# Optimization experiments

Measured on AMD Instinct MI355X. Metric: run time of the kernel, lower is better.

The kernel has to match this reference:

```python
import jax, jax.numpy as jnp
import numpy as np

NUM_CODES = 8192
LATENT_DIM = 256
BETA = 0.25
EPS_NORM = 1e-12  # F.normalize eps


def setup_inputs() -> dict:
    key = jax.random.key(0)
    k1, k2 = jax.random.split(key)
    z = jax.random.normal(k1, (8, LATENT_DIM, 32, 32), dtype=jnp.float32)
    # embedding initialized uniform(-1/K, 1/K); use that scale for realism
    codebook = jax.random.uniform(k2, (NUM_CODES, LATENT_DIM), dtype=jnp.float32,
                                  minval=-1.0 / NUM_CODES, maxval=1.0 / NUM_CODES)
    return {"z": z, "codebook": codebook}


def reference(z, codebook):
    # forward re-normalizes the codebook rows (F.normalize dim=1)
    norm = jnp.sqrt(jnp.sum(codebook * codebook, axis=1, keepdims=True))
    w = codebook / jnp.maximum(norm, EPS_NORM)                      # [K, D]

    z_perm = jnp.transpose(z, (0, 2, 3, 1))                          # [B, H, W, D]
    B, H, W, D = z_perm.shape
    zf = z_perm.reshape(-1, D)                                       # [N, D]

    # squared euclidean distances: ||z||^2 + ||w||^2 - 2 z w^T
    d = (jnp.sum(zf * zf, axis=1, keepdims=True)
         + jnp.sum(w * w, axis=1)
         - 2.0 * jnp.einsum('nd,kd->nk', zf, w))                     # [N, K]
    idx = jnp.argmin(d, axis=1)                                      # [N] int

    z_q = w[idx].reshape(B, H, W, D)                                 # gather

    # commitment + codebook loss
    loss = (jnp.mean((jax.lax.stop_gradient(z_q) - z_perm) ** 2)
            + BETA * jnp.mean((z_q - jax.lax.stop_gradient(z_perm)) ** 2))

    # straight-through estimator
    z_q = z_perm + jax.lax.stop_gradient(z_q - z_perm)

    # perplexity from codeword usage histogram (== mean of one-hots)
    N = idx.shape[0]
    counts = jnp.zeros((NUM_CODES,), dtype=jnp.float32).at[idx].add(1.0)
    avg_probs = counts / N
    perplexity = jnp.exp(-jnp.sum(avg_probs * jnp.log(avg_probs + 1e-10)))

    z_q = jnp.transpose(z_q, (0, 3, 1, 2))                           # back to NCHW
    return (z_q, idx, loss, perplexity)
```

## Files before the change

kernel.cpp:

```cpp
#include <hip/hip_runtime.h>
#include <hip/hip_bf16.h>
#include <math.h>

#define KC 8192
#define DD 256
#define NP 8192
#define ZQ_ELEMS 2097152
#define MARGIN_S 2.5e-4f
#define NPART 32

#define OFF_ABIG 0u
#define OFF_BBIG 8388608u
#define OFF_NRM  16777216u
#define OFF_WSQ  16809984u
#define OFF_ZSQ  16842752u
#define OFF_PV1  16875520u
#define OFF_PV2  17924096u
#define OFF_PK1  18972672u
#define OFF_LOSSP 20021248u
#define OFF_IDX  20025344u
#define OFF_FLAG 20058112u
#define OFF_HIST 20090880u
#define OFF_PACK 20123648u
#define OFF_LIST 20189184u
#define OFF_NFLG 20221952u

typedef __attribute__((ext_vector_type(8))) short bf16x8;
typedef __attribute__((ext_vector_type(4))) float f32x4;
typedef __attribute__((address_space(3))) void as3_void;
typedef const __attribute__((address_space(1))) void as1_cvoid;

#define GLOAD16(g, l) __builtin_amdgcn_global_load_lds((as1_cvoid*)(g), (as3_void*)(l), 16, 0, 0)

__device__ inline double waveReduceD(double v) {
#pragma unroll
    for (int off = 32; off; off >>= 1) v += __shfl_down(v, off, 64);
    return v;
}

static __device__ inline unsigned short f2bf(float f) {
    __hip_bfloat16 h = __float2bfloat16(f);
    return *(unsigned short*)&h;
}
static __device__ inline float bf2f(unsigned short u) {
    unsigned v = ((unsigned)u) << 16;
    float f;
    __builtin_memcpy(&f, &v, 4);
    return f;
}

__global__ __launch_bounds__(256) void prep(
    const float* __restrict__ cb, const float* __restrict__ z,
    unsigned short* __restrict__ Bbig, unsigned short* __restrict__ Abig,
    float* __restrict__ nrm, float* __restrict__ wsq, float* __restrict__ zsq,
    int* __restrict__ hist, int* __restrict__ nflag) {
    __shared__ double lred[4];
    __shared__ float mh;
    int bid = blockIdx.x, t = threadIdx.x;
    int lane = t & 63, wid = t >> 6;
    if (bid < KC) {
        int k = bid;
        if (k < 32) hist[k * 256 + t] = 0;
        if (k == 32 && t == 0) *nflag = 0;
        float c = cb[k * DD + t];
        double s = waveReduceD((double)c * (double)c);
        if (lane == 0) lred[wid] = s;
        __syncthreads();
        if (t == 0) {
            double tot = lred[0] + lred[1] + lred[2] + lred[3];
            float nf = sqrtf((float)tot);
            mh = fmaxf(nf, 1e-12f);
        }
        __syncthreads();
        float wv = c / mh;
        unsigned short hi = f2bf(wv);
        unsigned short lo = f2bf(wv - bf2f(hi));
        Bbig[k * 512 + t] = hi;
        Bbig[k * 512 + 256 + t] = lo;
        if (t == 0) nrm[k] = mh;
        __syncthreads();
        double s2 = waveReduceD((double)wv * (double)wv);
        if (lane == 0) lred[wid] = s2;
        __syncthreads();
        if (t == 0) wsq[k] = (float)(lred[0] + lred[1] + lred[2] + lred[3]);
    } else {
        int n = bid - KC;
        int b = n >> 10, hw = n & 1023;
        float v = z[(b * DD + t) * 1024 + hw];
        unsigned short hi = f2bf(v);
        unsigned short lo = f2bf(v - bf2f(hi));
        Abig[n * 512 + t] = hi;
        Abig[n * 512 + 256 + t] = lo;
        double s = waveReduceD((double)v * (double)v);
        if (lane == 0) lred[wid] = s;
        __syncthreads();
        if (t == 0) zsq[n] = (float)(lred[0] + lred[1] + lred[2] + lred[3]);
    }
}

__global__ __launch_bounds__(512, 2) void gemm_top2(
    const unsigned short* __restrict__ Abig, const unsigned short* __restrict__ Bbig,
    const float* __restrict__ wsq,
    float* __restrict__ pv1, float* __restrict__ pv2, int* __restrict__ pk1) {
    __shared__ unsigned short sAB[65536];

    int t = threadIdx.x;
    int l = t & 63, w = t >> 6;
    int wm = w >> 2, wn = w & 3;
    int kc0 = blockIdx.y * 256;
    int n0 = blockIdx.x * 256;

    int row0 = t >> 2;
    int lsw = (((t & 3) ^ ((row0 >> 1) & 3)) << 3);
    int subsw = (((l >> 4) ^ ((l >> 1) & 3)) << 3);

#define STAGE(kt_) do {                                                        \
    int p_ = (kt_) >> 3;                                                       \
    int zo_ = (p_ == 2 ? 256 : 0) + ((kt_) & 7) * 32;                          \
    int wo_ = (p_ == 1 ? 256 : 0) + ((kt_) & 7) * 32;                          \
    int b_ = ((kt_) & 3) * 16384;                                              \
    GLOAD16(Bbig + (size_t)(kc0 + row0) * 512 + wo_ + lsw, &sAB[b_ + t * 8]);  \
    GLOAD16(Bbig + (size_t)(kc0 + row0 + 128) * 512 + wo_ + lsw, &sAB[b_ + 4096 + t * 8]); \
    GLOAD16(Abig + (size_t)(n0 + row0) * 512 + zo_ + lsw, &sAB[b_ + 8192 + t * 8]); \
    GLOAD16(Abig + (size_t)(n0 + row0 + 128) * 512 + zo_ + lsw, &sAB[b_ + 12288 + t * 8]); \
} while (0)

    f32x4 acc[8][4];
#pragma unroll
    for (int mf = 0; mf < 8; ++mf) {
#pragma unroll
        for (int r = 0; r < 4; ++r) {
            float hv = -0.5f * wsq[kc0 + wm * 128 + mf * 16 + ((l >> 4) << 2) + r];
#pragma unroll
            for (int nf = 0; nf < 4; ++nf) acc[mf][nf][r] = hv;
        }
    }

#define KBODY(bufbase) do {                                                    \
    bf16x8 af[8], bfr[4];                                                      \
    _Pragma("unroll")                                                          \
    for (int mf = 0; mf < 8; ++mf)                                             \
        af[mf] = *(const bf16x8*)&sAB[(bufbase) + (wm * 128 + mf * 16 + (l & 15)) * 32 + subsw]; \
    _Pragma("unroll")                                                          \
    for (int nf = 0; nf < 4; ++nf)                                             \
        bfr[nf] = *(const bf16x8*)&sAB[(bufbase) + 8192 + (wn * 64 + nf * 16 + (l & 15)) * 32 + subsw]; \
    __builtin_amdgcn_s_setprio(1);                                             \
    _Pragma("unroll")                                                          \
    for (int mf = 0; mf < 8; ++mf)                                             \
        _Pragma("unroll")                                                      \
        for (int nf = 0; nf < 4; ++nf)                                         \
            acc[mf][nf] = __builtin_amdgcn_mfma_f32_16x16x32_bf16(af[mf], bfr[nf], acc[mf][nf], 0, 0, 0); \
    __builtin_amdgcn_s_setprio(0);                                             \
} while (0)

    STAGE(0);
    STAGE(1);
    STAGE(2);
    asm volatile("s_waitcnt vmcnt(8)" ::: "memory");
    __builtin_amdgcn_s_barrier();
    asm volatile("" ::: "memory");

    for (int kt = 0; kt < 21; ++kt) {
        STAGE(kt + 3);
        KBODY((kt & 3) * 16384);
        asm volatile("s_waitcnt vmcnt(8)" ::: "memory");
        __builtin_amdgcn_s_barrier();
        asm volatile("" ::: "memory");
    }
    KBODY(1 * 16384);
    asm volatile("s_waitcnt vmcnt(4)" ::: "memory");
    __builtin_amdgcn_s_barrier();
    asm volatile("" ::: "memory");
    KBODY(2 * 16384);
    asm volatile("s_waitcnt vmcnt(0)" ::: "memory");
    __builtin_amdgcn_s_barrier();
    asm volatile("" ::: "memory");
    KBODY(3 * 16384);

    float v1[4], v2[4];
    int k1[4];
#pragma unroll
    for (int nf = 0; nf < 4; ++nf) { v1[nf] = 3.4e38f; v2[nf] = 3.4e38f; k1[nf] = 0; }
#pragma unroll
    for (int mf = 0; mf < 8; ++mf) {
#pragma unroll
        for (int r = 0; r < 4; ++r) {
            int code = kc0 + wm * 128 + mf * 16 + ((l >> 4) << 2) + r;
#pragma unroll
            for (int nf = 0; nf < 4; ++nf) {
                float dv = -acc[mf][nf][r];
                bool lt = dv < v1[nf];
                v2[nf] = fminf(v2[nf], fmaxf(v1[nf], dv));
                v1[nf] = fminf(v1[nf], dv);
                k1[nf] = lt ? code : k1[nf];
            }
        }
    }
#pragma unroll
    for (int nf = 0; nf < 4; ++nf) {
#pragma unroll
        for (int mask = 16; mask <= 32; mask <<= 1) {
            float ov1 = __shfl_xor(v1[nf], mask, 64);
            float ov2 = __shfl_xor(v2[nf], mask, 64);
            int ok1 = __shfl_xor(k1[nf], mask, 64);
            bool take = (ov1 < v1[nf]) || (ov1 == v1[nf] && ok1 < k1[nf]);
            if (take) { v2[nf] = fminf(v1[nf], ov2); v1[nf] = ov1; k1[nf] = ok1; }
            else v2[nf] = fminf(v2[nf], ov1);
        }
    }
    __syncthreads();
    float* sv1 = (float*)sAB;
    float* sv2 = sv1 + 512;
    int* sk1 = (int*)(sv2 + 512);
    if ((l >> 4) == 0) {
#pragma unroll
        for (int nf = 0; nf < 4; ++nf) {
            int col = wn * 64 + nf * 16 + l;
            sv1[col * 2 + wm] = v1[nf];
            sv2[col * 2 + wm] = v2[nf];
            sk1[col * 2 + wm] = k1[nf];
        }
    }
    __syncthreads();
    if (t < 256) {
        float a1 = sv1[t * 2], b1 = sv1[t * 2 + 1];
        float a2 = sv2[t * 2], b2 = sv2[t * 2 + 1];
        int ak = sk1[t * 2], bk = sk1[t * 2 + 1];
        bool tb = (b1 < a1) || (b1 == a1 && bk < ak);
        float w1 = tb ? b1 : a1;
        int wk = tb ? bk : ak;
        float w2 = tb ? fminf(b2, a1) : fminf(a2, b1);
        pv1[blockIdx.y * NP + n0 + t] = w1;
        pv2[blockIdx.y * NP + n0 + t] = w2;
        pk1[blockIdx.y * NP + n0 + t] = wk;
    }
#undef STAGE
#undef KBODY
}

__global__ __launch_bounds__(256) void merge_top2(
    const float* __restrict__ pv1, const float* __restrict__ pv2,
    const int* __restrict__ pk1, int* __restrict__ idxw, int* __restrict__ flag,
    int* __restrict__ list, int* __restrict__ nflag,
    unsigned long long* __restrict__ packed) {
    int n = blockIdx.x * 256 + threadIdx.x;
    float gv1 = 3.4e38f, gv2 = 3.4e38f;
    int gk1 = 0;
#pragma unroll
    for (int ct = 0; ct < NPART; ++ct) {
        float v1 = pv1[ct * NP + n];
        if (v1 < gv1) {
            gv2 = fminf(gv1, pv2[ct * NP + n]);
            gv1 = v1;
            gk1 = pk1[ct * NP + n];
        } else {
            gv2 = fminf(gv2, v1);
        }
    }
    idxw[n] = gk1;
    int f = (gv2 - gv1 < MARGIN_S) ? 1 : 0;
    flag[n] = f;
    if (f) {
        packed[n] = 0xFFFFFFFFFFFFFFFFull;
        int pos = atomicAdd(nflag, 1);
        list[pos] = n;
    }
}

__global__ __launch_bounds__(256) void rescore_par(
    const float* __restrict__ z, const float* __restrict__ cb,
    const float* __restrict__ nrm, const float* __restrict__ wsq,
    const float* __restrict__ zsq, const int* __restrict__ list,
    const int* __restrict__ nflag, unsigned long long* __restrict__ packed) {
    __shared__ float sz[256];
    int nf = *nflag;
    int t = threadIdx.x;
    int lane = t & 63, wv = t >> 6;
    for (int ii = blockIdx.x; ii < nf; ii += 64) {
        int n = list[ii];
        int b = n >> 10, hw = n & 1023;
        __syncthreads();
        sz[t] = z[(b * DD + t) * 1024 + hw];
        __syncthreads();
        float4 zr = ((const float4*)sz)[lane];
        float zq = zsq[n];
        unsigned long long best = 0xFFFFFFFFFFFFFFFFull;
        int kbase = blockIdx.y * 256 + wv * 64;
        for (int j = 0; j < 64; ++j) {
            int k = kbase + j;
            float4 cc = *(const float4*)&cb[(size_t)k * DD + lane * 4];
            float p = (zr.x * cc.x + zr.y * cc.y) + (zr.z * cc.z + zr.w * cc.w);
#pragma unroll
            for (int off = 32; off; off >>= 1) p += __shfl_xor(p, off, 64);
            float dot = p / nrm[k];
            float dv = (zq + wsq[k]) - 2.0f * dot;
            unsigned bits = __float_as_uint(dv);
            bits = (bits & 0x80000000u) ? ~bits : (bits | 0x80000000u);
            unsigned long long pk = ((unsigned long long)bits << 32) | (unsigned)k;
            best = best < pk ? best : pk;
        }
        if (lane == 0) atomicMin(packed + n, best);
    }
}

__global__ __launch_bounds__(256) void fix_hist(
    const int* __restrict__ flag, const unsigned long long* __restrict__ packed,
    int* __restrict__ idxw, float* __restrict__ out, int* __restrict__ hist) {
    int n = blockIdx.x * 256 + threadIdx.x;
    int k = flag[n] ? (int)(packed[n] & 0xFFFFFFFFull) : idxw[n];
    idxw[n] = k;
    out[ZQ_ELEMS + n] = (float)k;
    atomicAdd(&hist[k], 1);
}

__global__ __launch_bounds__(256) void gather_loss(
    const float* __restrict__ z, const float* __restrict__ cb,
    const float* __restrict__ nrm, const int* __restrict__ idxw,
    float* __restrict__ out, double* __restrict__ lossp) {
    __shared__ double lred[4];
    int t = threadIdx.x;
    int base = (blockIdx.x * 256 + t) * 16;
    double s = 0.0;
#pragma unroll
    for (int q = 0; q < 4; ++q) {
        int e = base + q * 4;
        int b = e >> 18, d = (e >> 10) & 255, hw = e & 1023;
        int n = (b << 10) + hw;
        float4 zv = *(const float4*)&z[e];
        float o[4];
#pragma unroll
        for (int j = 0; j < 4; ++j) {
            int k = idxw[n + j];
            o[j] = cb[k * DD + d] / nrm[k];
        }
        *(float4*)&out[e] = make_float4(o[0], o[1], o[2], o[3]);
        float d0 = o[0] - zv.x, d1 = o[1] - zv.y, d2 = o[2] - zv.z, d3 = o[3] - zv.w;
        s += (double)(d0 * d0) + (double)(d1 * d1) + (double)(d2 * d2) + (double)(d3 * d3);
    }
    s = waveReduceD(s);
    int lane = t & 63, wid = t >> 6;
    if (lane == 0) lred[wid] = s;
    __syncthreads();
    if (t == 0) lossp[blockIdx.x] = lred[0] + lred[1] + lred[2] + lred[3];
}

__global__ __launch_bounds__(256) void finalize_kernel(
    const int* __restrict__ hist, const double* __restrict__ lossp,
    float* __restrict__ out) {
    __shared__ double lred[4];
    __shared__ double lsum;
    int t = threadIdx.x;
    int lane = t & 63, wid = t >> 6;
    double ls = lossp[t] + lossp[t + 256];
    ls = waveReduceD(ls);
    if (lane == 0) lred[wid] = ls;
    __syncthreads();
    if (t == 0) lsum = lred[0] + lred[1] + lred[2] + lred[3];
    __syncthreads();
    double s = 0.0;
    for (int i = t; i < KC; i += 256) {
        float p = (float)hist[i] * (1.0f / 8192.0f);
        float lg = logf(p + 1e-10f);
        s += (double)(p * lg);
    }
    s = waveReduceD(s);
    if (lane == 0) lred[wid] = s;
    __syncthreads();
    if (t == 0) {
        double tot = lred[0] + lred[1] + lred[2] + lred[3];
        float m = (float)(lsum / (double)ZQ_ELEMS);
        out[ZQ_ELEMS + NP] = m + 0.25f * m;
        out[ZQ_ELEMS + NP + 1] = expf(-(float)tot);
    }
}

extern "C" void kernel_launch(void* const* d_in, const int* in_sizes, int n_in,
                              void* d_out, int out_size, void* d_ws, size_t ws_size,
                              hipStream_t stream) {
    const float* z = (const float*)d_in[0];
    const float* cb = (const float*)d_in[1];
    float* out = (float*)d_out;
    char* ws = (char*)d_ws;

    unsigned short* Abig = (unsigned short*)(ws + OFF_ABIG);
    unsigned short* Bbig = (unsigned short*)(ws + OFF_BBIG);
    float* nrm = (float*)(ws + OFF_NRM);
    float* wsq = (float*)(ws + OFF_WSQ);
    float* zsq = (float*)(ws + OFF_ZSQ);
    float* pv1 = (float*)(ws + OFF_PV1);
    float* pv2 = (float*)(ws + OFF_PV2);
    int* pk1 = (int*)(ws + OFF_PK1);
    int* idxw = (int*)(ws + OFF_IDX);
    int* flag = (int*)(ws + OFF_FLAG);
    int* hist = (int*)(ws + OFF_HIST);
    double* lossp = (double*)(ws + OFF_LOSSP);
    unsigned long long* packed = (unsigned long long*)(ws + OFF_PACK);
    int* list = (int*)(ws + OFF_LIST);
    int* nflag = (int*)(ws + OFF_NFLG);

    prep<<<2 * KC, 256, 0, stream>>>(cb, z, Bbig, Abig, nrm, wsq, zsq, hist, nflag);
    gemm_top2<<<dim3(32, NPART), 512, 0, stream>>>(Abig, Bbig, wsq, pv1, pv2, pk1);
    merge_top2<<<NP / 256, 256, 0, stream>>>(pv1, pv2, pk1, idxw, flag, list, nflag, packed);
    rescore_par<<<dim3(64, 32), 256, 0, stream>>>(z, cb, nrm, wsq, zsq, list, nflag, packed);
    fix_hist<<<NP / 256, 256, 0, stream>>>(flag, packed, idxw, out, hist);
    gather_loss<<<ZQ_ELEMS / (256 * 16), 256, 0, stream>>>(z, cb, nrm, idxw, out, lossp);
    finalize_kernel<<<1, 256, 0, stream>>>(hist, lossp, out);
}
```

Baseline: 217.4 us.

## Interleave LDS fragment loads, global staging and MFMA in four barriered phases

The GEMM k-tile body is split into four phases. Each phase loads two A fragments from LDS, issues one quarter of the next tile's global-to-LDS copies, and runs 8 MFMAs, with s_barrier and setprio around each phase to keep waves in lockstep. The goal is to spread global-load issue and LDS reads across the MFMA stream and lower register pressure from holding all eight A fragments at once. The cost is many more barriers per tile, which could stall waves. Separately, the prep kernel derives the normalized row's squared norm as tot/mh^2 instead of running a second block reduction.

Measured after the change: 215.6 us. No clear change (-0.8%).

```diff
diff --git a/kernel.cpp b/kernel.cpp
--- a/kernel.cpp
+++ b/kernel.cpp
@@ -70,6 +70,8 @@
             double tot = lred[0] + lred[1] + lred[2] + lred[3];
             float nf = sqrtf((float)tot);
             mh = fmaxf(nf, 1e-12f);
+            nrm[k] = mh;
+            wsq[k] = (float)(tot / ((double)mh * (double)mh));
         }
         __syncthreads();
         float wv = c / mh;
@@ -77,12 +79,6 @@
         unsigned short lo = f2bf(wv - bf2f(hi));
         Bbig[k * 512 + t] = hi;
         Bbig[k * 512 + 256 + t] = lo;
-        if (t == 0) nrm[k] = mh;
-        __syncthreads();
-        double s2 = waveReduceD((double)wv * (double)wv);
-        if (lane == 0) lred[wid] = s2;
-        __syncthreads();
-        if (t == 0) wsq[k] = (float)(lred[0] + lred[1] + lred[2] + lred[3]);
     } else {
         int n = bid - KC;
         int b = n >> 10, hw = n & 1023;
@@ -114,15 +110,66 @@
     int lsw = (((t & 3) ^ ((row0 >> 1) & 3)) << 3);
     int subsw = (((l >> 4) ^ ((l >> 1) & 3)) << 3);
 
-#define STAGE(kt_) do {                                                        \
+#define STAGE1(kt_, piece) do {                                                \
     int p_ = (kt_) >> 3;                                                       \
     int zo_ = (p_ == 2 ? 256 : 0) + ((kt_) & 7) * 32;                          \
     int wo_ = (p_ == 1 ? 256 : 0) + ((kt_) & 7) * 32;                          \
     int b_ = ((kt_) & 3) * 16384;                                              \
-    GLOAD16(Bbig + (size_t)(kc0 + row0) * 512 + wo_ + lsw, &sAB[b_ + t * 8]);  \
-    GLOAD16(Bbig + (size_t)(kc0 + row0 + 128) * 512 + wo_ + lsw, &sAB[b_ + 4096 + t * 8]); \
-    GLOAD16(Abig + (size_t)(n0 + row0) * 512 + zo_ + lsw, &sAB[b_ + 8192 + t * 8]); \
-    GLOAD16(Abig + (size_t)(n0 + row0 + 128) * 512 + zo_ + lsw, &sAB[b_ + 12288 + t * 8]); \
+    if ((piece) == 0) GLOAD16(Bbig + (size_t)(kc0 + row0) * 512 + wo_ + lsw, &sAB[b_ + t * 8]); \
+    else if ((piece) == 1) GLOAD16(Bbig + (size_t)(kc0 + row0 + 128) * 512 + wo_ + lsw, &sAB[b_ + 4096 + t * 8]); \
+    else if ((piece) == 2) GLOAD16(Abig + (size_t)(n0 + row0) * 512 + zo_ + lsw, &sAB[b_ + 8192 + t * 8]); \
+    else GLOAD16(Abig + (size_t)(n0 + row0 + 128) * 512 + zo_ + lsw, &sAB[b_ + 12288 + t * 8]); \
+} while (0)
+
+#define STAGE4(kt_) do { STAGE1(kt_, 0); STAGE1(kt_, 1); STAGE1(kt_, 2); STAGE1(kt_, 3); } while (0)
+
+#define LDA(bb, mf) (*(const bf16x8*)&sAB[(bb) + (wm * 128 + (mf) * 16 + (l & 15)) * 32 + subsw])
+#define LDB(bb, nf) (*(const bf16x8*)&sAB[(bb) + 8192 + (wn * 64 + (nf) * 16 + (l & 15)) * 32 + subsw])
+
+#define MFMA8(m0) do {                                                         \
+    _Pragma("unroll")                                                          \
+    for (int nf_ = 0; nf_ < 4; ++nf_)                                          \
+        acc[m0][nf_] = __builtin_amdgcn_mfma_f32_16x16x32_bf16(aA_, bfr[nf_], acc[m0][nf_], 0, 0, 0); \
+    _Pragma("unroll")                                                          \
+    for (int nf_ = 0; nf_ < 4; ++nf_)                                          \
+        acc[(m0) + 1][nf_] = __builtin_amdgcn_mfma_f32_16x16x32_bf16(aB_, bfr[nf_], acc[(m0) + 1][nf_], 0, 0, 0); \
+} while (0)
+
+#define KTILE(kt_, STEN, VMLINE) do {                                          \
+    const int bb_ = ((kt_) & 3) * 16384;                                       \
+    bf16x8 bfr[4];                                                             \
+    bf16x8 aA_, aB_;                                                           \
+                                                                  \
+    aA_ = LDA(bb_, 0); aB_ = LDA(bb_, 1);                                      \
+    bfr[0] = LDB(bb_, 0); bfr[1] = LDB(bb_, 1);                                \
+    bfr[2] = LDB(bb_, 2); bfr[3] = LDB(bb_, 3);                                \
+    if (STEN) STAGE1((kt_) + 3, 0);                                            \
+    __builtin_amdgcn_s_barrier();                                              \
+    asm volatile("s_waitcnt lgkmcnt(0)" ::: "memory");                         \
+    __builtin_amdgcn_s_setprio(1); MFMA8(0); __builtin_amdgcn_s_setprio(0);    \
+    __builtin_amdgcn_s_barrier();                                              \
+                                                                  \
+    aA_ = LDA(bb_, 2); aB_ = LDA(bb_, 3);                                      \
+    if (STEN) STAGE1((kt_) + 3, 1);                                            \
+    __builtin_amdgcn_s_barrier();                                              \
+    asm volatile("s_waitcnt lgkmcnt(0)" ::: "memory");                         \
+    __builtin_amdgcn_s_setprio(1); MFMA8(2); __builtin_amdgcn_s_setprio(0);    \
+    __builtin_amdgcn_s_barrier();                                              \
+                                                                  \
+    aA_ = LDA(bb_, 4); aB_ = LDA(bb_, 5);                                      \
+    if (STEN) STAGE1((kt_) + 3, 2);                                            \
+    __builtin_amdgcn_s_barrier();                                              \
+    asm volatile("s_waitcnt lgkmcnt(0)" ::: "memory");                         \
+    __builtin_amdgcn_s_setprio(1); MFMA8(4); __builtin_amdgcn_s_setprio(0);    \
+    __builtin_amdgcn_s_barrier();                                              \
+                                                                  \
+    aA_ = LDA(bb_, 6); aB_ = LDA(bb_, 7);                                      \
+    if (STEN) STAGE1((kt_) + 3, 3);                                            \
+    VMLINE;                                                                    \
+    __builtin_amdgcn_s_barrier();                                              \
+    asm volatile("s_waitcnt lgkmcnt(0)" ::: "memory");                         \
+    __builtin_amdgcn_s_setprio(1); MFMA8(6); __builtin_amdgcn_s_setprio(0);    \
+    __builtin_amdgcn_s_barrier();                                              \
 } while (0)
 
     f32x4 acc[8][4];
@@ -136,46 +183,18 @@
         }
     }
 
-#define KBODY(bufbase) do {                                                    \
-    bf16x8 af[8], bfr[4];                                                      \
-    _Pragma("unroll")                                                          \
-    for (int mf = 0; mf < 8; ++mf)                                             \
-        af[mf] = *(const bf16x8*)&sAB[(bufbase) + (wm * 128 + mf * 16 + (l & 15)) * 32 + subsw]; \
-    _Pragma("unroll")                                                          \
-    for (int nf = 0; nf < 4; ++nf)                                             \
-        bfr[nf] = *(const bf16x8*)&sAB[(bufbase) + 8192 + (wn * 64 + nf * 16 + (l & 15)) * 32 + subsw]; \
-    __builtin_amdgcn_s_setprio(1);                                             \
-    _Pragma("unroll")                                                          \
-    for (int mf = 0; mf < 8; ++mf)                                             \
-        _Pragma("unroll")                                                      \
-        for (int nf = 0; nf < 4; ++nf)                                         \
-            acc[mf][nf] = __builtin_amdgcn_mfma_f32_16x16x32_bf16(af[mf], bfr[nf], acc[mf][nf], 0, 0, 0); \
-    __builtin_amdgcn_s_setprio(0);                                             \
-} while (0)
-
-    STAGE(0);
-    STAGE(1);
-    STAGE(2);
+    STAGE4(0);
+    STAGE4(1);
+    STAGE4(2);
     asm volatile("s_waitcnt vmcnt(8)" ::: "memory");
     __builtin_amdgcn_s_barrier();
-    asm volatile("" ::: "memory");
 
     for (int kt = 0; kt < 21; ++kt) {
-        STAGE(kt + 3);
-        KBODY((kt & 3) * 16384);
-        asm volatile("s_waitcnt vmcnt(8)" ::: "memory");
-        __builtin_amdgcn_s_barrier();
-        asm volatile("" ::: "memory");
-    }
-    KBODY(1 * 16384);
-    asm volatile("s_waitcnt vmcnt(4)" ::: "memory");
-    __builtin_amdgcn_s_barrier();
-    asm volatile("" ::: "memory");
-    KBODY(2 * 16384);
-    asm volatile("s_waitcnt vmcnt(0)" ::: "memory");
-    __builtin_amdgcn_s_barrier();
-    asm volatile("" ::: "memory");
-    KBODY(3 * 16384);
+        KTILE(kt, 1, asm volatile("s_waitcnt vmcnt(8)" ::: "memory"));
+    }
+    KTILE(21, 0, asm volatile("s_waitcnt vmcnt(4)" ::: "memory"));
+    KTILE(22, 0, asm volatile("s_waitcnt vmcnt(0)" ::: "memory"));
+    KTILE(23, 0, ((void)0));
 
     float v1[4], v2[4];
     int k1[4];
@@ -234,8 +253,12 @@
         pv2[blockIdx.y * NP + n0 + t] = w2;
         pk1[blockIdx.y * NP + n0 + t] = wk;
     }
-#undef STAGE
-#undef KBODY
+#undef STAGE1
+#undef STAGE4
+#undef LDA
+#undef LDB
+#undef MFMA8
+#undef KTILE
 }
 
 __global__ __launch_bounds__(256) void merge_top2(
```

## Tile-transpose z in prep, drop zsq/idx/flag buffers, fuse fix_hist into gather

Applied to the files above, without the earlier changes.

The z half of prep now loads 64x64 tiles through padded shared memory, so both the global reads and the Abig writes are coalesced. It also needs far fewer blocks than the old one-block-per-row scheme, which read strided columns. wsq is derived from the first norm reduction, removing a second block reduction per codebook row. zsq moves into rescore_par, and merge_top2 writes either the winning index or a sentinel into packed. This removes the idx and flag arrays and the fix_hist kernel, whose index output and histogram atomics now run inside gather_loss. The cost is extra per-wave reduction work in rescore and histogram atomics inside the gather kernel.

Result: faster. 208.6 us (-4.1%).

```diff
diff --git a/kernel.cpp b/kernel.cpp
--- a/kernel.cpp
+++ b/kernel.cpp
@@ -13,13 +13,10 @@
 #define OFF_BBIG 8388608u
 #define OFF_NRM  16777216u
 #define OFF_WSQ  16809984u
-#define OFF_ZSQ  16842752u
 #define OFF_PV1  16875520u
 #define OFF_PV2  17924096u
 #define OFF_PK1  18972672u
 #define OFF_LOSSP 20021248u
-#define OFF_IDX  20025344u
-#define OFF_FLAG 20058112u
 #define OFF_HIST 20090880u
 #define OFF_PACK 20123648u
 #define OFF_LIST 20189184u
@@ -52,13 +49,14 @@
 __global__ __launch_bounds__(256) void prep(
     const float* __restrict__ cb, const float* __restrict__ z,
     unsigned short* __restrict__ Bbig, unsigned short* __restrict__ Abig,
-    float* __restrict__ nrm, float* __restrict__ wsq, float* __restrict__ zsq,
+    float* __restrict__ nrm, float* __restrict__ wsq,
     int* __restrict__ hist, int* __restrict__ nflag) {
-    __shared__ double lred[4];
-    __shared__ float mh;
+    __shared__ float tile[64][65];
     int bid = blockIdx.x, t = threadIdx.x;
     int lane = t & 63, wid = t >> 6;
     if (bid < KC) {
+        __shared__ double lred[4];
+        __shared__ float mh;
         int k = bid;
         if (k < 32) hist[k * 256 + t] = 0;
         if (k == 32 && t == 0) *nflag = 0;
@@ -70,6 +68,8 @@
             double tot = lred[0] + lred[1] + lred[2] + lred[3];
             float nf = sqrtf((float)tot);
             mh = fmaxf(nf, 1e-12f);
+            nrm[k] = mh;
+            wsq[k] = (float)(tot / ((double)mh * (double)mh));
         }
         __syncthreads();
         float wv = c / mh;
@@ -77,24 +77,26 @@
         unsigned short lo = f2bf(wv - bf2f(hi));
         Bbig[k * 512 + t] = hi;
         Bbig[k * 512 + 256 + t] = lo;
-        if (t == 0) nrm[k] = mh;
+    } else {
+        int zb = bid - KC;
+        int b = zb >> 6, ht = (zb >> 2) & 15, dt = zb & 3;
+        int hw0 = ht * 64, d0 = dt * 64;
+#pragma unroll
+        for (int i = 0; i < 16; ++i) {
+            int dl = wid * 16 + i;
+            tile[dl][lane] = z[(size_t)(b * DD + d0 + dl) * 1024 + hw0 + lane];
+        }
         __syncthreads();
-        double s2 = waveReduceD((double)wv * (double)wv);
-        if (lane == 0) lred[wid] = s2;
-        __syncthreads();
-        if (t == 0) wsq[k] = (float)(lred[0] + lred[1] + lred[2] + lred[3]);
-    } else {
-        int n = bid - KC;
-        int b = n >> 10, hw = n & 1023;
-        float v = z[(b * DD + t) * 1024 + hw];
-        unsigned short hi = f2bf(v);
-        unsigned short lo = f2bf(v - bf2f(hi));
-        Abig[n * 512 + t] = hi;
-        Abig[n * 512 + 256 + t] = lo;
-        double s = waveReduceD((double)v * (double)v);
-        if (lane == 0) lred[wid] = s;
-        __syncthreads();
-        if (t == 0) zsq[n] = (float)(lred[0] + lred[1] + lred[2] + lred[3]);
+#pragma unroll
+        for (int i = 0; i < 16; ++i) {
+            int nl = wid * 16 + i;
+            float v = tile[lane][nl];
+            unsigned short hi = f2bf(v);
+            unsigned short lo = f2bf(v - bf2f(hi));
+            size_t base = (size_t)(b * 1024 + hw0 + nl) * 512 + d0 + lane;
+            Abig[base] = hi;
+            Abig[base + 256] = lo;
+        }
     }
 }
 
@@ -240,8 +242,7 @@
 
 __global__ __launch_bounds__(256) void merge_top2(
     const float* __restrict__ pv1, const float* __restrict__ pv2,
-    const int* __restrict__ pk1, int* __restrict__ idxw, int* __restrict__ flag,
-    int* __restrict__ list, int* __restrict__ nflag,
+    const int* __restrict__ pk1, int* __restrict__ list, int* __restrict__ nflag,
     unsigned long long* __restrict__ packed) {
     int n = blockIdx.x * 256 + threadIdx.x;
     float gv1 = 3.4e38f, gv2 = 3.4e38f;
@@ -257,11 +258,9 @@
             gv2 = fminf(gv2, v1);
         }
     }
-    idxw[n] = gk1;
     int f = (gv2 - gv1 < MARGIN_S) ? 1 : 0;
-    flag[n] = f;
+    packed[n] = f ? 0xFFFFFFFFFFFFFFFFull : (unsigned long long)(unsigned)gk1;
     if (f) {
-        packed[n] = 0xFFFFFFFFFFFFFFFFull;
         int pos = atomicAdd(nflag, 1);
         list[pos] = n;
     }
@@ -270,8 +269,8 @@
 __global__ __launch_bounds__(256) void rescore_par(
     const float* __restrict__ z, const float* __restrict__ cb,
     const float* __restrict__ nrm, const float* __restrict__ wsq,
-    const float* __restrict__ zsq, const int* __restrict__ list,
-    const int* __restrict__ nflag, unsigned long long* __restrict__ packed) {
+    const int* __restrict__ list, const int* __restrict__ nflag,
+    unsigned long long* __restrict__ packed) {
     __shared__ float sz[256];
     int nf = *nflag;
     int t = threadIdx.x;
@@ -283,7 +282,11 @@
         sz[t] = z[(b * DD + t) * 1024 + hw];
         __syncthreads();
         float4 zr = ((const float4*)sz)[lane];
-        float zq = zsq[n];
+        double zqd = (double)zr.x * zr.x + (double)zr.y * zr.y
+                   + (double)zr.z * zr.z + (double)zr.w * zr.w;
+#pragma unroll
+        for (int off = 32; off; off >>= 1) zqd += __shfl_xor(zqd, off, 64);
+        float zq = (float)zqd;
         unsigned long long best = 0xFFFFFFFFFFFFFFFFull;
         int kbase = blockIdx.y * 256 + wv * 64;
         for (int j = 0; j < 64; ++j) {
@@ -303,20 +306,10 @@
     }
 }
 
-__global__ __launch_bounds__(256) void fix_hist(
-    const int* __restrict__ flag, const unsigned long long* __restrict__ packed,
-    int* __restrict__ idxw, float* __restrict__ out, int* __restrict__ hist) {
-    int n = blockIdx.x * 256 + threadIdx.x;
-    int k = flag[n] ? (int)(packed[n] & 0xFFFFFFFFull) : idxw[n];
-    idxw[n] = k;
-    out[ZQ_ELEMS + n] = (float)k;
-    atomicAdd(&hist[k], 1);
-}
-
 __global__ __launch_bounds__(256) void gather_loss(
     const float* __restrict__ z, const float* __restrict__ cb,
-    const float* __restrict__ nrm, const int* __restrict__ idxw,
-    float* __restrict__ out, double* __restrict__ lossp) {
+    const float* __restrict__ nrm, const unsigned long long* __restrict__ packed,
+    float* __restrict__ out, double* __restrict__ lossp, int* __restrict__ hist) {
     __shared__ double lred[4];
     int t = threadIdx.x;
     int base = (blockIdx.x * 256 + t) * 16;
@@ -328,12 +321,20 @@
         int n = (b << 10) + hw;
         float4 zv = *(const float4*)&z[e];
         float o[4];
+        int ks[4];
 #pragma unroll
         for (int j = 0; j < 4; ++j) {
-            int k = idxw[n + j];
-            o[j] = cb[k * DD + d] / nrm[k];
+            ks[j] = (int)(packed[n + j] & 0xFFFFFFFFull);
+            o[j] = cb[ks[j] * DD + d] / nrm[ks[j]];
         }
         *(float4*)&out[e] = make_float4(o[0], o[1], o[2], o[3]);
+        if (d == 0) {
+#pragma unroll
+            for (int j = 0; j < 4; ++j) {
+                out[ZQ_ELEMS + n + j] = (float)ks[j];
+                atomicAdd(&hist[ks[j]], 1);
+            }
+        }
         float d0 = o[0] - zv.x, d1 = o[1] - zv.y, d2 = o[2] - zv.z, d3 = o[3] - zv.w;
         s += (double)(d0 * d0) + (double)(d1 * d1) + (double)(d2 * d2) + (double)(d3 * d3);
     }
@@ -386,23 +387,19 @@
     unsigned short* Bbig = (unsigned short*)(ws + OFF_BBIG);
     float* nrm = (float*)(ws + OFF_NRM);
     float* wsq = (float*)(ws + OFF_WSQ);
-    float* zsq = (float*)(ws + OFF_ZSQ);
     float* pv1 = (float*)(ws + OFF_PV1);
     float* pv2 = (float*)(ws + OFF_PV2);
     int* pk1 = (int*)(ws + OFF_PK1);
-    int* idxw = (int*)(ws + OFF_IDX);
-    int* flag = (int*)(ws + OFF_FLAG);
     int* hist = (int*)(ws + OFF_HIST);
     double* lossp = (double*)(ws + OFF_LOSSP);
     unsigned long long* packed = (unsigned long long*)(ws + OFF_PACK);
     int* list = (int*)(ws + OFF_LIST);
     int* nflag = (int*)(ws + OFF_NFLG);
 
-    prep<<<2 * KC, 256, 0, stream>>>(cb, z, Bbig, Abig, nrm, wsq, zsq, hist, nflag);
+    prep<<<KC + 512, 256, 0, stream>>>(cb, z, Bbig, Abig, nrm, wsq, hist, nflag);
     gemm_top2<<<dim3(32, NPART), 512, 0, stream>>>(Abig, Bbig, wsq, pv1, pv2, pk1);
-    merge_top2<<<NP / 256, 256, 0, stream>>>(pv1, pv2, pk1, idxw, flag, list, nflag, packed);
-    rescore_par<<<dim3(64, 32), 256, 0, stream>>>(z, cb, nrm, wsq, zsq, list, nflag, packed);
-    fix_hist<<<NP / 256, 256, 0, stream>>>(flag, packed, idxw, out, hist);
-    gather_loss<<<ZQ_ELEMS / (256 * 16), 256, 0, stream>>>(z, cb, nrm, idxw, out, lossp);
+    merge_top2<<<NP / 256, 256, 0, stream>>>(pv1, pv2, pk1, list, nflag, packed);
+    rescore_par<<<dim3(64, 32), 256, 0, stream>>>(z, cb, nrm, wsq, list, nflag, packed);
+    gather_loss<<<ZQ_ELEMS / (256 * 16), 256, 0, stream>>>(z, cb, nrm, packed, out, lossp, hist);
     finalize_kernel<<<1, 256, 0, stream>>>(hist, lossp, out);
 }
```
